# Kernel tuning notes

Hardware: AMD Instinct MI355X
Metric: run time of the kernel (lower is better)

Reference implementation:

```python
import jax, jax.numpy as jnp
import numpy as np

NUM_LAYERS = 4
HIDDEN = 512
HEADS = 8
DK = HIDDEN // HEADS
REPR_IN = 53
REPR_HID = 32
LN_EPS = 1e-5


def _mask_by_1dmask(x, mask):
    # x: [B,H,L,L], mask: [B,L] bool
    pair = mask[:, :, None] & mask[:, None, :]          # [B,L,L]
    masked = jnp.where(pair[:, None, :, :], x, -jnp.inf)
    all_inf = jnp.all(masked == -jnp.inf, axis=-1, keepdims=True)
    return jnp.where(all_inf, 0.0, masked)


def _layernorm(x, g, b):
    mu = jnp.mean(x, axis=-1, keepdims=True)
    var = jnp.mean((x - mu) ** 2, axis=-1, keepdims=True)
    return (x - mu) * jax.lax.rsqrt(var + LN_EPS) * g + b


def _attn_block(x, mask, refCov, Wq, bq, Wk, bk, Wv, bv, Wo, bo,
                Wr1, br1, Wr2, br2, ln_g, ln_b):
    B, L, h = x.shape
    residual = x
    q = (x @ Wq + bq).reshape(B, L, HEADS, DK).transpose(0, 2, 1, 3)  # [B,H,L,dk]
    k = (x @ Wk + bk).reshape(B, L, HEADS, DK).transpose(0, 2, 1, 3)
    v = (x @ Wv + bv).reshape(B, L, HEADS, DK).transpose(0, 2, 1, 3)
    scores = jnp.einsum('bhid,bhjd->bhij', q, k) / np.sqrt(DK).astype(np.float32)
    scores = _mask_by_1dmask(scores, mask)
    attn_w = jax.nn.softmax(scores, axis=-1)
    # per-pair MLP bias: [B,L,L,53] -> [B,L,L,H] -> [B,H,L,L]
    ref = jax.nn.relu(refCov @ Wr1 + br1) @ Wr2 + br2
    ref = ref.transpose(0, 3, 1, 2)
    ref = _mask_by_1dmask(ref, mask)
    ref_w = jax.nn.softmax(ref, axis=-1)
    comb = attn_w + ref_w
    comb = comb / jnp.sum(comb, axis=-1, keepdims=True)
    out = jnp.einsum('bhij,bhjd->bhid', comb, v)
    out = out.transpose(0, 2, 1, 3).reshape(B, L, h)
    out = out @ Wo + bo
    return _layernorm(residual + out, ln_g, ln_b)


def setup_inputs() -> dict:
    key = jax.random.key(0)
    ks = jax.random.split(key, 20)
    B, L = 8, 384
    s = 0.02
    inp = {
        'x': jax.random.normal(ks[0], (B, L, HIDDEN), jnp.float32),
        'mask': jax.random.randint(ks[1], (B, L), 0, 2) > 0,
        'refCov': jax.random.normal(ks[2], (B, L, L, REPR_IN), jnp.float32),
        'Wq': jax.random.normal(ks[3], (NUM_LAYERS, HIDDEN, HIDDEN)) * s,
        'bq': jnp.zeros((NUM_LAYERS, HIDDEN)),
        'Wk': jax.random.normal(ks[4], (NUM_LAYERS, HIDDEN, HIDDEN)) * s,
        'bk': jnp.zeros((NUM_LAYERS, HIDDEN)),
        'Wv': jax.random.normal(ks[5], (NUM_LAYERS, HIDDEN, HIDDEN)) * s,
        'bv': jnp.zeros((NUM_LAYERS, HIDDEN)),
        'Wo': jax.random.normal(ks[6], (NUM_LAYERS, HIDDEN, HIDDEN)) * s,
        'bo': jnp.zeros((NUM_LAYERS, HIDDEN)),
        'Wr1': jax.random.normal(ks[7], (NUM_LAYERS, REPR_IN, REPR_HID)) * 0.1,
        'br1': jnp.zeros((NUM_LAYERS, REPR_HID)),
        'Wr2': jax.random.normal(ks[8], (NUM_LAYERS, REPR_HID, HEADS)) * 0.1,
        'br2': jnp.zeros((NUM_LAYERS, HEADS)),
        'ln_g': jnp.ones((NUM_LAYERS, HIDDEN)),
        'ln_b': jnp.zeros((NUM_LAYERS, HIDDEN)),
        'fn_g': jnp.ones((HIDDEN,)),
        'fn_b': jnp.zeros((HIDDEN,)),
    }
    return inp


def reference(x, mask, refCov, Wq, bq, Wk, bk, Wv, bv, Wo, bo,
              Wr1, br1, Wr2, br2, ln_g, ln_b, fn_g, fn_b):
    # process_node_feature packs flat nodes into [B,L,h] with zeros at padding;
    # equivalent here to zeroing padded positions of x.
    h = x * mask[:, :, None].astype(x.dtype)
    for i in range(NUM_LAYERS):
        h = _attn_block(h, mask, refCov, Wq[i], bq[i], Wk[i], bk[i],
                        Wv[i], bv[i], Wo[i], bo[i], Wr1[i], br1[i],
                        Wr2[i], br2[i], ln_g[i], ln_b[i])
    h = _layernorm(h, fn_g, fn_b)
    return jnp.sum(h * mask[:, :, None].astype(h.dtype), axis=1)  # [B, HIDDEN]
```

## Files before the change

### kernel.cpp

```cpp
#include <hip/hip_runtime.h>
#include <hip/hip_bf16.h>
#include <cstdint>

constexpr int LSEQ  = 384;
constexpr int BATCH = 8;
constexpr int HID   = 512;
constexpr int NHEAD = 8;
constexpr int DKH   = 64;
constexpr int NLAY  = 4;
constexpr int BL    = BATCH * LSEQ;
constexpr int LL2   = LSEQ * LSEQ;
constexpr int BH    = BATCH * NHEAD;

typedef __bf16 bf16x8 __attribute__((ext_vector_type(8)));
typedef float  f32x4  __attribute__((ext_vector_type(4)));
typedef unsigned short ushort_t;

__device__ inline bf16x8 load_frag(const void* p) {
    uint4 u = *reinterpret_cast<const uint4*>(p);
    return __builtin_bit_cast(bf16x8, u);
}
__device__ inline bf16x8 zero_frag() {
    uint4 u = {0u, 0u, 0u, 0u};
    return __builtin_bit_cast(bf16x8, u);
}
__device__ inline f32x4 mfma16(bf16x8 a, bf16x8 b, f32x4 c) {
    return __builtin_amdgcn_mfma_f32_16x16x32_bf16(a, b, c, 0, 0, 0);
}
__device__ inline float b2f(__hip_bfloat16 v) { return __bfloat162float(v); }
__device__ inline ushort_t bfbits(float f) {
    __hip_bfloat16 b = __float2bfloat16(f);
    return *(ushort_t*)&b;
}

__global__ __launch_bounds__(1024) void mask_norm_kernel(
    const unsigned char* __restrict__ raw, unsigned char* __restrict__ m)
{
    __shared__ int fl;
    const int tid = threadIdx.x;
    if (tid == 0) fl = 0;
    __syncthreads();
    int f = 0;
    for (int i = tid; i < BL; i += 1024) {
        const unsigned char v = raw[i];
        if (v > 1) f |= 1;
        if (v && (i & 3)) f |= 2;
        if (v && ((i & 7) == 4)) f |= 4;
        if (v && ((i & 3) <= 1)) f |= 8;
    }
    if (f) atomicOr(&fl, f);
    __syncthreads();
    const int ff = fl;
    int stride, off;
    if (ff & 1) { if (ff & 8) { stride = 2; off = 0; } else { stride = 4; off = 2; } }
    else if (ff & 2) { stride = 1; off = 0; }
    else if (ff & 4) { stride = 4; off = 0; }
    else             { stride = 8; off = 0; }
    for (int i = tid; i < BL; i += 1024)
        m[i] = raw[(size_t)i * stride + off] ? 1 : 0;
}

__global__ __launch_bounds__(256) void wconv_kernel(
    const float* __restrict__ Wq, const float* __restrict__ Wk,
    const float* __restrict__ Wv, const float* __restrict__ Wo,
    ushort_t* __restrict__ WTqkv, ushort_t* __restrict__ WTo)
{
    __shared__ float tile[32][33];
    const int t = blockIdx.x;
    const int ml = t >> 8;
    const int rest = t & 255;
    const int mi = ml >> 2, l = ml & 3;
    const int tk = (rest & 15) * 32;
    const int tn = (rest >> 4) * 32;
    const float* W = (mi == 0) ? Wq : (mi == 1) ? Wk : (mi == 2) ? Wv : Wo;
    const float* src = W + (size_t)l * HID * HID;
    const int c = threadIdx.x & 31, r = threadIdx.x >> 5;
    for (int rr = r; rr < 32; rr += 8)
        tile[rr][c] = src[(size_t)(tk + rr) * HID + tn + c];
    __syncthreads();
    ushort_t* dst = (mi < 3)
        ? WTqkv + ((size_t)l * 1536 + mi * 512) * HID
        : WTo   + (size_t)l * HID * HID;
    for (int rr = r; rr < 32; rr += 8)
        dst[(size_t)(tn + rr) * HID + tk + c] = bfbits(tile[c][rr]);
}

__global__ __launch_bounds__(256) void refw_kernel(
    const float* __restrict__ Wr1, const float* __restrict__ Wr2,
    ushort_t* __restrict__ W1T, ushort_t* __restrict__ W2T)
{
    const int tid = blockIdx.x * 256 + threadIdx.x;
    if (tid < 4 * 32 * 64) {
        const int l = tid >> 11, rem = tid & 2047;
        const int n = rem >> 6, k = rem & 63;
        W1T[tid] = (k < 53) ? bfbits(Wr1[(l * 53 + k) * 32 + n]) : (ushort_t)0;
    } else if (tid < 4 * 32 * 64 + 4 * 16 * 32) {
        const int t2 = tid - 8192;
        const int l = t2 >> 9, rem = t2 & 511;
        const int n = rem >> 5, k = rem & 31;
        W2T[t2] = (n < 8) ? bfbits(Wr2[(l * 32 + k) * 8 + n]) : (ushort_t)0;
    }
}

__global__ __launch_bounds__(256) void pack_kernel(
    const float* __restrict__ x, const unsigned char* __restrict__ mask,
    float* __restrict__ h, __hip_bfloat16* __restrict__ hb)
{
    const int idx = blockIdx.x * 256 + threadIdx.x;
    const int row = idx >> 9;
    const float v = mask[row] ? x[idx] : 0.f;
    h[idx] = v;
    hb[idx] = __float2bfloat16(v);
}

__global__ __launch_bounds__(256) void refmlp_kernel(
    const float* __restrict__ refCov,
    const ushort_t* __restrict__ W1T, const float* __restrict__ br1,
    const ushort_t* __restrict__ W2T, const float* __restrict__ br2,
    __hip_bfloat16* __restrict__ refL)
{
    __shared__ ushort_t smem[256 * 56];

    const int tid = threadIdx.x;
    const int w = tid >> 6, lane = tid & 63;
    const int lr = lane & 15, quad = lane >> 4;
    const size_t p0 = (size_t)blockIdx.x * 256;
    const int b = (int)(p0 / LL2);
    const int rem0 = (int)(p0 - (size_t)b * LL2);

    const float4* src4 = reinterpret_cast<const float4*>(refCov + p0 * 53);
    for (int f = tid; f < 3392; f += 256) {
        float4 v = src4[f];
        const int e = f * 4;
        #pragma unroll
        for (int k = 0; k < 4; ++k) {
            const int g = e + k;
            const int row = g / 53;
            const int col = g - row * 53;
            smem[row * 56 + col] = bfbits(((const float*)&v)[k]);
        }
    }
    smem[tid * 56 + 53] = 0;
    smem[tid * 56 + 54] = 0;
    smem[tid * 56 + 55] = 0;
    __syncthreads();

    bf16x8 afr[4][2];
    #pragma unroll
    for (int mi = 0; mi < 4; ++mi) {
        const ushort_t* rp = smem + (w * 64 + mi * 16 + lr) * 56;
        afr[mi][0] = load_frag(rp + quad * 8);
        afr[mi][1] = (quad < 3) ? load_frag(rp + 32 + quad * 8) : zero_frag();
    }
    __syncthreads();

    ushort_t* C1w = smem + w * 2560;

    #pragma unroll
    for (int l = 0; l < NLAY; ++l) {
        const float bias0 = br1[l * 32 + lr];
        const float bias1 = br1[l * 32 + 16 + lr];
        const float bias2 = br2[l * 8 + (lr & 7)];
        bf16x8 w1f[2][2];
        #pragma unroll
        for (int ni = 0; ni < 2; ++ni)
            #pragma unroll
            for (int ks = 0; ks < 2; ++ks)
                w1f[ni][ks] = load_frag(W1T + ((l * 32 + ni * 16 + lr) * 64) + ks * 32 + quad * 8);
        bf16x8 w2f = load_frag(W2T + (l * 16 + lr) * 32 + quad * 8);

        f32x4 acc[4][2];
        #pragma unroll
        for (int mi = 0; mi < 4; ++mi) {
            acc[mi][0] = (f32x4){bias0, bias0, bias0, bias0};
            acc[mi][1] = (f32x4){bias1, bias1, bias1, bias1};
        }
        #pragma unroll
        for (int mi = 0; mi < 4; ++mi) {
            acc[mi][0] = mfma16(afr[mi][0], w1f[0][0], acc[mi][0]);
            acc[mi][0] = mfma16(afr[mi][1], w1f[0][1], acc[mi][0]);
            acc[mi][1] = mfma16(afr[mi][0], w1f[1][0], acc[mi][1]);
            acc[mi][1] = mfma16(afr[mi][1], w1f[1][1], acc[mi][1]);
        }
        #pragma unroll
        for (int mi = 0; mi < 4; ++mi)
            #pragma unroll
            for (int ni = 0; ni < 2; ++ni)
                #pragma unroll
                for (int r = 0; r < 4; ++r)
                    C1w[(mi * 16 + quad * 4 + r) * 40 + ni * 16 + lr] =
                        bfbits(fmaxf(acc[mi][ni][r], 0.f));

        #pragma unroll
        for (int mi = 0; mi < 4; ++mi) {
            bf16x8 a2 = load_frag(C1w + (mi * 16 + lr) * 40 + quad * 8);
            f32x4 a = (f32x4){bias2, bias2, bias2, bias2};
            a = mfma16(a2, w2f, a);
            if (lr < 8) {
                uint2 pk;
                pk.x = (unsigned)bfbits(a[0]) | ((unsigned)bfbits(a[1]) << 16);
                pk.y = (unsigned)bfbits(a[2]) | ((unsigned)bfbits(a[3]) << 16);
                const size_t plane = ((size_t)(l * 8 + b) * 8 + lr) * LL2;
                *reinterpret_cast<uint2*>((ushort_t*)refL + plane + rem0 +
                                          w * 64 + mi * 16 + quad * 4) = pk;
            }
        }
    }
}

__global__ __launch_bounds__(256) void gemm_qkv_kernel(
    const __hip_bfloat16* __restrict__ A,
    const __hip_bfloat16* __restrict__ BT,
    const float* __restrict__ bq, const float* __restrict__ bk,
    const float* __restrict__ bv,
    __hip_bfloat16* __restrict__ q, __hip_bfloat16* __restrict__ kk,
    __hip_bfloat16* __restrict__ vT)
{
    const int bm = blockIdx.x % (BL / 64);
    const int bn = blockIdx.x / (BL / 64);
    const int wv = threadIdx.x >> 6;
    const int lane = threadIdx.x & 63;
    const int lr = lane & 15, quad = lane >> 4;
    const int m0 = bm * 64 + (wv & 1) * 32;
    const int n0g = bn * 64 + (wv >> 1) * 32;
    f32x4 acc[2][2];
    #pragma unroll
    for (int i = 0; i < 2; ++i)
        #pragma unroll
        for (int j = 0; j < 2; ++j) acc[i][j] = (f32x4){0.f, 0.f, 0.f, 0.f};
    const __hip_bfloat16* a0p = A + (size_t)(m0 + lr) * HID;
    const __hip_bfloat16* a1p = A + (size_t)(m0 + 16 + lr) * HID;
    const __hip_bfloat16* b0p = BT + (size_t)(n0g + lr) * HID;
    const __hip_bfloat16* b1p = BT + (size_t)(n0g + 16 + lr) * HID;
    #pragma unroll 4
    for (int k0 = 0; k0 < HID; k0 += 32) {
        const int ka = k0 + quad * 8;
        bf16x8 a0 = load_frag(a0p + ka);
        bf16x8 a1 = load_frag(a1p + ka);
        bf16x8 b0 = load_frag(b0p + ka);
        bf16x8 b1 = load_frag(b1p + ka);
        acc[0][0] = mfma16(a0, b0, acc[0][0]);
        acc[0][1] = mfma16(a0, b1, acc[0][1]);
        acc[1][0] = mfma16(a1, b0, acc[1][0]);
        acc[1][1] = mfma16(a1, b1, acc[1][1]);
    }
    const int mat = n0g >> 9;
    const float* bias = (mat == 0) ? bq : (mat == 1) ? bk : bv;
    const float scale = (mat == 0) ? 0.125f : 1.0f;
    __hip_bfloat16* outp = (mat == 0) ? q : (mat == 1) ? kk : vT;
    #pragma unroll
    for (int mi = 0; mi < 2; ++mi)
        #pragma unroll
        for (int ni = 0; ni < 2; ++ni)
            #pragma unroll
            for (int r = 0; r < 4; ++r) {
                const int m = m0 + mi * 16 + quad * 4 + r;
                const int ng = n0g + ni * 16 + lr;
                const int n = ng & 511;
                float v = (acc[mi][ni][r] + bias[n]) * scale;
                const int bb = m / LSEQ, ii = m % LSEQ;
                const int hh = n >> 6, d = n & 63;
                if (mat == 2)
                    outp[((size_t)(bb * NHEAD + hh) * DKH + d) * LSEQ + ii] = __float2bfloat16(v);
                else
                    outp[((size_t)(bb * NHEAD + hh) * LSEQ + ii) * DKH + d] = __float2bfloat16(v);
            }
}

__global__ __launch_bounds__(256) void gemm_oproj_kernel(
    const __hip_bfloat16* __restrict__ A,
    const __hip_bfloat16* __restrict__ BT,
    const float* __restrict__ bias,
    float* __restrict__ outf)
{
    const int bm = blockIdx.x % (BL / 64);
    const int bn = blockIdx.x / (BL / 64);
    const int wv = threadIdx.x >> 6;
    const int lane = threadIdx.x & 63;
    const int lr = lane & 15, quad = lane >> 4;
    const int m0 = bm * 64 + (wv & 1) * 32;
    const int n0 = bn * 64 + (wv >> 1) * 32;
    f32x4 acc[2][2];
    #pragma unroll
    for (int i = 0; i < 2; ++i)
        #pragma unroll
        for (int j = 0; j < 2; ++j) acc[i][j] = (f32x4){0.f, 0.f, 0.f, 0.f};
    const __hip_bfloat16* a0p = A + (size_t)(m0 + lr) * HID;
    const __hip_bfloat16* a1p = A + (size_t)(m0 + 16 + lr) * HID;
    const __hip_bfloat16* b0p = BT + (size_t)(n0 + lr) * HID;
    const __hip_bfloat16* b1p = BT + (size_t)(n0 + 16 + lr) * HID;
    #pragma unroll 4
    for (int k0 = 0; k0 < HID; k0 += 32) {
        const int ka = k0 + quad * 8;
        bf16x8 a0 = load_frag(a0p + ka);
        bf16x8 a1 = load_frag(a1p + ka);
        bf16x8 b0 = load_frag(b0p + ka);
        bf16x8 b1 = load_frag(b1p + ka);
        acc[0][0] = mfma16(a0, b0, acc[0][0]);
        acc[0][1] = mfma16(a0, b1, acc[0][1]);
        acc[1][0] = mfma16(a1, b0, acc[1][0]);
        acc[1][1] = mfma16(a1, b1, acc[1][1]);
    }
    #pragma unroll
    for (int mi = 0; mi < 2; ++mi)
        #pragma unroll
        for (int ni = 0; ni < 2; ++ni)
            #pragma unroll
            for (int r = 0; r < 4; ++r) {
                const int m = m0 + mi * 16 + quad * 4 + r;
                const int n = n0 + ni * 16 + lr;
                outf[(size_t)m * HID + n] = acc[mi][ni][r] + bias[n];
            }
}

__global__ __launch_bounds__(256) void attn_fused_kernel(
    const __hip_bfloat16* __restrict__ Q,
    const __hip_bfloat16* __restrict__ Km,
    const __hip_bfloat16* __restrict__ VT,
    const __hip_bfloat16* __restrict__ refl,
    const unsigned char* __restrict__ mask,
    __hip_bfloat16* __restrict__ AO)
{
    __shared__ __align__(16) ushort_t Pl[32 * 392];
    __shared__ float redm_s[2][2][16], redm_r[2][2][16];
    __shared__ float reds_s[2][2][16], reds_r[2][2][16];

    const int bh = blockIdx.x / 12;
    const int i0 = (blockIdx.x % 12) * 32;
    const int b  = bh >> 3, hh = bh & 7;
    const int w = threadIdx.x >> 6, lane = threadIdx.x & 63;
    const int s = w & 1, h2 = w >> 1;
    const int lr = lane & 15, quad = lane >> 4;

    const __hip_bfloat16* qb = Q  + (size_t)bh * LSEQ * DKH;
    const __hip_bfloat16* kb = Km + (size_t)bh * LSEQ * DKH;
    const unsigned char* mrow = mask + b * LSEQ;

    f32x4 acc[12];
    #pragma unroll
    for (int nt = 0; nt < 12; ++nt) acc[nt] = (f32x4){0.f, 0.f, 0.f, 0.f};
    #pragma unroll
    for (int k0 = 0; k0 < DKH; k0 += 32) {
        const int ka = k0 + quad * 8;
        bf16x8 a = load_frag(qb + (size_t)(i0 + s * 16 + lr) * DKH + ka);
        #pragma unroll
        for (int nt = 0; nt < 12; ++nt) {
            bf16x8 bf = load_frag(kb + (size_t)(h2 * 192 + nt * 16 + lr) * DKH + ka);
            acc[nt] = mfma16(a, bf, acc[nt]);
        }
    }

    bool vm[12];
    #pragma unroll
    for (int nt = 0; nt < 12; ++nt)
        vm[nt] = mrow[h2 * 192 + nt * 16 + lr] != 0;

    const __hip_bfloat16* rbase = refl + (size_t)bh * LL2 +
                                  (size_t)(i0 + s * 16) * LSEQ + h2 * 192;
    float rv[12][4];
    #pragma unroll
    for (int nt = 0; nt < 12; ++nt)
        #pragma unroll
        for (int r = 0; r < 4; ++r)
            rv[nt][r] = b2f(rbase[(size_t)(quad * 4 + r) * LSEQ + nt * 16 + lr]);

    float ms[4], mr2[4];
    #pragma unroll
    for (int r = 0; r < 4; ++r) { ms[r] = -1e30f; mr2[r] = -1e30f; }
    #pragma unroll
    for (int nt = 0; nt < 12; ++nt)
        #pragma unroll
        for (int r = 0; r < 4; ++r) {
            acc[nt][r] = vm[nt] ? acc[nt][r] : -1e30f;
            rv[nt][r]  = vm[nt] ? rv[nt][r]  : -1e30f;
            ms[r]  = fmaxf(ms[r],  acc[nt][r]);
            mr2[r] = fmaxf(mr2[r], rv[nt][r]);
        }
    #pragma unroll
    for (int off = 8; off > 0; off >>= 1)
        #pragma unroll
        for (int r = 0; r < 4; ++r) {
            ms[r]  = fmaxf(ms[r],  __shfl_xor(ms[r],  off));
            mr2[r] = fmaxf(mr2[r], __shfl_xor(mr2[r], off));
        }
    if (lr == 0)
        #pragma unroll
        for (int r = 0; r < 4; ++r) {
            redm_s[s][h2][quad * 4 + r] = ms[r];
            redm_r[s][h2][quad * 4 + r] = mr2[r];
        }
    __syncthreads();
    #pragma unroll
    for (int r = 0; r < 4; ++r) {
        ms[r]  = fmaxf(redm_s[s][0][quad * 4 + r], redm_s[s][1][quad * 4 + r]);
        mr2[r] = fmaxf(redm_r[s][0][quad * 4 + r], redm_r[s][1][quad * 4 + r]);
    }

    float Ss[4] = {0.f, 0.f, 0.f, 0.f}, Sr[4] = {0.f, 0.f, 0.f, 0.f};
    #pragma unroll
    for (int nt = 0; nt < 12; ++nt)
        #pragma unroll
        for (int r = 0; r < 4; ++r) {
            acc[nt][r] = __expf(acc[nt][r] - ms[r]);  Ss[r] += acc[nt][r];
            rv[nt][r]  = __expf(rv[nt][r]  - mr2[r]); Sr[r] += rv[nt][r];
        }
    #pragma unroll
    for (int off = 8; off > 0; off >>= 1)
        #pragma unroll
        for (int r = 0; r < 4; ++r) {
            Ss[r] += __shfl_xor(Ss[r], off);
            Sr[r] += __shfl_xor(Sr[r], off);
        }
    if (lr == 0)
        #pragma unroll
        for (int r = 0; r < 4; ++r) {
            reds_s[s][h2][quad * 4 + r] = Ss[r];
            reds_r[s][h2][quad * 4 + r] = Sr[r];
        }
    __syncthreads();

    float cs[4], cr[4], rm[4];
    #pragma unroll
    for (int r = 0; r < 4; ++r) {
        const float SsF = reds_s[s][0][quad * 4 + r] + reds_s[s][1][quad * 4 + r];
        const float SrF = reds_r[s][0][quad * 4 + r] + reds_r[s][1][quad * 4 + r];
        cs[r] = 0.5f / SsF;
        cr[r] = 0.5f / SrF;
        rm[r] = mrow[i0 + s * 16 + quad * 4 + r] ? 1.f : 0.f;
    }
    #pragma unroll
    for (int nt = 0; nt < 12; ++nt)
        #pragma unroll
        for (int r = 0; r < 4; ++r)
            Pl[(s * 16 + quad * 4 + r) * 392 + h2 * 192 + nt * 16 + lr] =
                bfbits((acc[nt][r] * cs[r] + rv[nt][r] * cr[r]) * rm[r]);
    __syncthreads();

    const __hip_bfloat16* vb = VT + (size_t)bh * DKH * LSEQ;
    f32x4 oa[2];
    oa[0] = (f32x4){0.f, 0.f, 0.f, 0.f};
    oa[1] = (f32x4){0.f, 0.f, 0.f, 0.f};
    #pragma unroll 4
    for (int k0 = 0; k0 < LSEQ; k0 += 32) {
        const int ka = k0 + quad * 8;
        bf16x8 a = load_frag(Pl + (s * 16 + lr) * 392 + ka);
        #pragma unroll
        for (int dt = 0; dt < 2; ++dt) {
            bf16x8 bf = load_frag(vb + (size_t)(h2 * 32 + dt * 16 + lr) * LSEQ + ka);
            oa[dt] = mfma16(a, bf, oa[dt]);
        }
    }
    #pragma unroll
    for (int dt = 0; dt < 2; ++dt)
        #pragma unroll
        for (int r = 0; r < 4; ++r)
            AO[(size_t)(b * LSEQ + i0 + s * 16 + quad * 4 + r) * HID +
               hh * DKH + h2 * 32 + dt * 16 + lr] = __float2bfloat16(oa[dt][r]);
}

__global__ __launch_bounds__(256) void ln_kernel(
    const float* __restrict__ resid, const float* __restrict__ proj,
    const float* __restrict__ g, const float* __restrict__ beta,
    float* __restrict__ outf, __hip_bfloat16* __restrict__ outb,
    const unsigned char* __restrict__ mask, int flags)
{
    const int row = blockIdx.x, tid = threadIdx.x;
    const size_t base = (size_t)row * HID;
    float x0 = resid[base + tid], x1 = resid[base + tid + 256];
    if (flags & 1) { x0 += proj[base + tid]; x1 += proj[base + tid + 256]; }
    float s = x0 + x1, s2 = x0 * x0 + x1 * x1;
    #pragma unroll
    for (int off = 32; off > 0; off >>= 1) {
        s += __shfl_xor(s, off);
        s2 += __shfl_xor(s2, off);
    }
    __shared__ float rs[4], rs2[4];
    if ((tid & 63) == 0) { rs[tid >> 6] = s; rs2[tid >> 6] = s2; }
    __syncthreads();
    s = rs[0] + rs[1] + rs[2] + rs[3];
    s2 = rs2[0] + rs2[1] + rs2[2] + rs2[3];
    const float mu = s * (1.f / HID);
    const float var = s2 * (1.f / HID) - mu * mu;
    const float rstd = rsqrtf(var + 1e-5f);
    float y0 = (x0 - mu) * rstd * g[tid] + beta[tid];
    float y1 = (x1 - mu) * rstd * g[tid + 256] + beta[tid + 256];
    if ((flags & 2) && !mask[row]) { y0 = 0.f; y1 = 0.f; }
    outf[base + tid] = y0;
    outf[base + tid + 256] = y1;
    if (flags & 4) {
        outb[base + tid] = __float2bfloat16(y0);
        outb[base + tid + 256] = __float2bfloat16(y1);
    }
}

__global__ __launch_bounds__(512) void reduce_kernel(
    const float* __restrict__ hf, float* __restrict__ out)
{
    const int b = blockIdx.x, c = threadIdx.x;
    float s = 0.f;
    for (int i = 0; i < LSEQ; ++i)
        s += hf[((size_t)(b * LSEQ + i)) * HID + c];
    out[b * HID + c] = s;
}

extern "C" void kernel_launch(void* const* d_in, const int* in_sizes, int n_in,
                              void* d_out, int out_size, void* d_ws, size_t ws_size,
                              hipStream_t stream)
{
    const float* x   = (const float*)d_in[0];
    const unsigned char* mraw = (const unsigned char*)d_in[1];
    const float* refCov = (const float*)d_in[2];
    const float* Wq = (const float*)d_in[3];
    const float* bq = (const float*)d_in[4];
    const float* Wk = (const float*)d_in[5];
    const float* bk = (const float*)d_in[6];
    const float* Wv = (const float*)d_in[7];
    const float* bv = (const float*)d_in[8];
    const float* Wo = (const float*)d_in[9];
    const float* bo = (const float*)d_in[10];
    const float* Wr1 = (const float*)d_in[11];
    const float* br1 = (const float*)d_in[12];
    const float* Wr2 = (const float*)d_in[13];
    const float* br2 = (const float*)d_in[14];
    const float* ln_g = (const float*)d_in[15];
    const float* ln_b = (const float*)d_in[16];
    const float* fn_g = (const float*)d_in[17];
    const float* fn_b = (const float*)d_in[18];
    float* outp = (float*)d_out;

    char* ws = (char*)d_ws;
    size_t off = 0;
    auto alloc = [&](size_t bytes) -> char* {
        char* p = ws + off;
        off += (bytes + 255) & ~(size_t)255;
        return p;
    };
    __hip_bfloat16* refL  = (__hip_bfloat16*)alloc((size_t)NLAY * BH * LL2 * 2);
    float*          h     = (float*)alloc((size_t)BL * HID * 4);
    __hip_bfloat16* hb    = (__hip_bfloat16*)alloc((size_t)BL * HID * 2);
    __hip_bfloat16* q     = (__hip_bfloat16*)alloc((size_t)BH * LSEQ * DKH * 2);
    __hip_bfloat16* kk    = (__hip_bfloat16*)alloc((size_t)BH * LSEQ * DKH * 2);
    __hip_bfloat16* vT    = (__hip_bfloat16*)alloc((size_t)BH * DKH * LSEQ * 2);
    float*          S     = (float*)alloc((size_t)BH * LL2 * 4);
    __hip_bfloat16* AO    = (__hip_bfloat16*)alloc((size_t)BL * HID * 2);
    float*          proj  = (float*)alloc((size_t)BL * HID * 4);
    ushort_t*       WTqkv = (ushort_t*)alloc((size_t)NLAY * 1536 * HID * 2);
    ushort_t*       WTo   = (ushort_t*)alloc((size_t)NLAY * HID * HID * 2);
    ushort_t*       W1T   = (ushort_t*)alloc((size_t)4 * 32 * 64 * 2);
    ushort_t*       W2T   = (ushort_t*)alloc((size_t)4 * 16 * 32 * 2);
    unsigned char*  msk   = (unsigned char*)alloc(BL);
    float*          hfin  = S;

    mask_norm_kernel<<<1, 1024, 0, stream>>>(mraw, msk);
    wconv_kernel<<<4096, 256, 0, stream>>>(Wq, Wk, Wv, Wo, WTqkv, WTo);
    refw_kernel<<<40, 256, 0, stream>>>(Wr1, Wr2, W1T, W2T);
    pack_kernel<<<6144, 256, 0, stream>>>(x, msk, h, hb);
    refmlp_kernel<<<4608, 256, 0, stream>>>(refCov, W1T, br1, W2T, br2, refL);

    for (int l = 0; l < NLAY; ++l) {
        const __hip_bfloat16* WTl = (const __hip_bfloat16*)(WTqkv + (size_t)l * 1536 * HID);
        const __hip_bfloat16* WTol = (const __hip_bfloat16*)(WTo + (size_t)l * HID * HID);
        gemm_qkv_kernel<<<1152, 256, 0, stream>>>(hb, WTl, bq + l * HID, bk + l * HID,
                                                  bv + l * HID, q, kk, vT);
        attn_fused_kernel<<<768, 256, 0, stream>>>(q, kk, vT,
                                                   refL + (size_t)l * BH * LL2, msk, AO);
        gemm_oproj_kernel<<<384, 256, 0, stream>>>(AO, WTol, bo + l * HID, proj);
        ln_kernel<<<3072, 256, 0, stream>>>(h, proj, ln_g + l * HID, ln_b + l * HID,
                                            h, hb, nullptr, 1 | 4);
    }
    ln_kernel<<<3072, 256, 0, stream>>>(h, nullptr, fn_g, fn_b, hfin, nullptr, msk, 2);
    reduce_kernel<<<8, 512, 0, stream>>>(hfin, outp);
}
```

Before: 840.2 us.

## Split attention block across eight waves instead of four

The fused attention kernel now launches 512 threads per block. The key dimension is split four ways (96 columns per wave) instead of two, and each wave produces 16 output dims instead of 32. This halves per-thread register arrays (score and ref tiles), which may raise occupancy and latency hiding for the ref loads. The cost is wider cross-wave reductions through shared memory, more waves syncing per block, and each Q fragment being loaded by more waves.

Result: no change. 830.0 us (-1.2%).

```diff
diff --git a/kernel.cpp b/kernel.cpp
--- a/kernel.cpp
+++ b/kernel.cpp
@@ -313,7 +313,7 @@
             }
 }
 
-__global__ __launch_bounds__(256) void attn_fused_kernel(
+__global__ __launch_bounds__(512) void attn_fused_kernel(
     const __hip_bfloat16* __restrict__ Q,
     const __hip_bfloat16* __restrict__ Km,
     const __hip_bfloat16* __restrict__ VT,
@@ -322,44 +322,44 @@
     __hip_bfloat16* __restrict__ AO)
 {
     __shared__ __align__(16) ushort_t Pl[32 * 392];
-    __shared__ float redm_s[2][2][16], redm_r[2][2][16];
-    __shared__ float reds_s[2][2][16], reds_r[2][2][16];
+    __shared__ float redm_s[2][4][16], redm_r[2][4][16];
+    __shared__ float reds_s[2][4][16], reds_r[2][4][16];
 
     const int bh = blockIdx.x / 12;
     const int i0 = (blockIdx.x % 12) * 32;
     const int b  = bh >> 3, hh = bh & 7;
     const int w = threadIdx.x >> 6, lane = threadIdx.x & 63;
-    const int s = w & 1, h2 = w >> 1;
+    const int s = w & 1, h4 = w >> 1;
     const int lr = lane & 15, quad = lane >> 4;
 
     const __hip_bfloat16* qb = Q  + (size_t)bh * LSEQ * DKH;
     const __hip_bfloat16* kb = Km + (size_t)bh * LSEQ * DKH;
     const unsigned char* mrow = mask + b * LSEQ;
 
-    f32x4 acc[12];
-    #pragma unroll
-    for (int nt = 0; nt < 12; ++nt) acc[nt] = (f32x4){0.f, 0.f, 0.f, 0.f};
+    f32x4 acc[6];
+    #pragma unroll
+    for (int nt = 0; nt < 6; ++nt) acc[nt] = (f32x4){0.f, 0.f, 0.f, 0.f};
     #pragma unroll
     for (int k0 = 0; k0 < DKH; k0 += 32) {
         const int ka = k0 + quad * 8;
         bf16x8 a = load_frag(qb + (size_t)(i0 + s * 16 + lr) * DKH + ka);
         #pragma unroll
-        for (int nt = 0; nt < 12; ++nt) {
-            bf16x8 bf = load_frag(kb + (size_t)(h2 * 192 + nt * 16 + lr) * DKH + ka);
+        for (int nt = 0; nt < 6; ++nt) {
+            bf16x8 bf = load_frag(kb + (size_t)(h4 * 96 + nt * 16 + lr) * DKH + ka);
             acc[nt] = mfma16(a, bf, acc[nt]);
         }
     }
 
-    bool vm[12];
-    #pragma unroll
-    for (int nt = 0; nt < 12; ++nt)
-        vm[nt] = mrow[h2 * 192 + nt * 16 + lr] != 0;
+    bool vm[6];
+    #pragma unroll
+    for (int nt = 0; nt < 6; ++nt)
+        vm[nt] = mrow[h4 * 96 + nt * 16 + lr] != 0;
 
     const __hip_bfloat16* rbase = refl + (size_t)bh * LL2 +
-                                  (size_t)(i0 + s * 16) * LSEQ + h2 * 192;
-    float rv[12][4];
-    #pragma unroll
-    for (int nt = 0; nt < 12; ++nt)
+                                  (size_t)(i0 + s * 16) * LSEQ + h4 * 96;
+    float rv[6][4];
+    #pragma unroll
+    for (int nt = 0; nt < 6; ++nt)
         #pragma unroll
         for (int r = 0; r < 4; ++r)
             rv[nt][r] = b2f(rbase[(size_t)(quad * 4 + r) * LSEQ + nt * 16 + lr]);
@@ -368,7 +368,7 @@
     #pragma unroll
     for (int r = 0; r < 4; ++r) { ms[r] = -1e30f; mr2[r] = -1e30f; }
     #pragma unroll
-    for (int nt = 0; nt < 12; ++nt)
+    for (int nt = 0; nt < 6; ++nt)
         #pragma unroll
         for (int r = 0; r < 4; ++r) {
             acc[nt][r] = vm[nt] ? acc[nt][r] : -1e30f;
@@ -386,19 +386,22 @@
     if (lr == 0)
         #pragma unroll
         for (int r = 0; r < 4; ++r) {
-            redm_s[s][h2][quad * 4 + r] = ms[r];
-            redm_r[s][h2][quad * 4 + r] = mr2[r];
+            redm_s[s][h4][quad * 4 + r] = ms[r];
+            redm_r[s][h4][quad * 4 + r] = mr2[r];
         }
     __syncthreads();
     #pragma unroll
     for (int r = 0; r < 4; ++r) {
-        ms[r]  = fmaxf(redm_s[s][0][quad * 4 + r], redm_s[s][1][quad * 4 + r]);
-        mr2[r] = fmaxf(redm_r[s][0][quad * 4 + r], redm_r[s][1][quad * 4 + r]);
+        const int x = quad * 4 + r;
+        ms[r]  = fmaxf(fmaxf(redm_s[s][0][x], redm_s[s][1][x]),
+                       fmaxf(redm_s[s][2][x], redm_s[s][3][x]));
+        mr2[r] = fmaxf(fmaxf(redm_r[s][0][x], redm_r[s][1][x]),
+                       fmaxf(redm_r[s][2][x], redm_r[s][3][x]));
     }
 
     float Ss[4] = {0.f, 0.f, 0.f, 0.f}, Sr[4] = {0.f, 0.f, 0.f, 0.f};
     #pragma unroll
-    for (int nt = 0; nt < 12; ++nt)
+    for (int nt = 0; nt < 6; ++nt)
         #pragma unroll
         for (int r = 0; r < 4; ++r) {
             acc[nt][r] = __expf(acc[nt][r] - ms[r]);  Ss[r] += acc[nt][r];
@@ -414,48 +417,44 @@
     if (lr == 0)
         #pragma unroll
         for (int r = 0; r < 4; ++r) {
-            reds_s[s][h2][quad * 4 + r] = Ss[r];
-            reds_r[s][h2][quad * 4 + r] = Sr[r];
+            reds_s[s][h4][quad * 4 + r] = Ss[r];
+            reds_r[s][h4][quad * 4 + r] = Sr[r];
         }
     __syncthreads();
 
     float cs[4], cr[4], rm[4];
     #pragma unroll
     for (int r = 0; r < 4; ++r) {
-        const float SsF = reds_s[s][0][quad * 4 + r] + reds_s[s][1][quad * 4 + r];
-        const float SrF = reds_r[s][0][quad * 4 + r] + reds_r[s][1][quad * 4 + r];
+        const int x = quad * 4 + r;
+        const float SsF = reds_s[s][0][x] + reds_s[s][1][x] +
+                          reds_s[s][2][x] + reds_s[s][3][x];
+        const float SrF = reds_r[s][0][x] + reds_r[s][1][x] +
+                          reds_r[s][2][x] + reds_r[s][3][x];
         cs[r] = 0.5f / SsF;
         cr[r] = 0.5f / SrF;
-        rm[r] = mrow[i0 + s * 16 + quad * 4 + r] ? 1.f : 0.f;
-    }
-    #pragma unroll
-    for (int nt = 0; nt < 12; ++nt)
+        rm[r] = mrow[i0 + s * 16 + x] ? 1.f : 0.f;
+    }
+    #pragma unroll
+    for (int nt = 0; nt < 6; ++nt)
         #pragma unroll
         for (int r = 0; r < 4; ++r)
-            Pl[(s * 16 + quad * 4 + r) * 392 + h2 * 192 + nt * 16 + lr] =
+            Pl[(s * 16 + quad * 4 + r) * 392 + h4 * 96 + nt * 16 + lr] =
                 bfbits((acc[nt][r] * cs[r] + rv[nt][r] * cr[r]) * rm[r]);
     __syncthreads();
 
     const __hip_bfloat16* vb = VT + (size_t)bh * DKH * LSEQ;
-    f32x4 oa[2];
-    oa[0] = (f32x4){0.f, 0.f, 0.f, 0.f};
-    oa[1] = (f32x4){0.f, 0.f, 0.f, 0.f};
+    f32x4 oa = (f32x4){0.f, 0.f, 0.f, 0.f};
     #pragma unroll 4
     for (int k0 = 0; k0 < LSEQ; k0 += 32) {
         const int ka = k0 + quad * 8;
         bf16x8 a = load_frag(Pl + (s * 16 + lr) * 392 + ka);
-        #pragma unroll
-        for (int dt = 0; dt < 2; ++dt) {
-            bf16x8 bf = load_frag(vb + (size_t)(h2 * 32 + dt * 16 + lr) * LSEQ + ka);
-            oa[dt] = mfma16(a, bf, oa[dt]);
-        }
-    }
-    #pragma unroll
-    for (int dt = 0; dt < 2; ++dt)
-        #pragma unroll
-        for (int r = 0; r < 4; ++r)
-            AO[(size_t)(b * LSEQ + i0 + s * 16 + quad * 4 + r) * HID +
-               hh * DKH + h2 * 32 + dt * 16 + lr] = __float2bfloat16(oa[dt][r]);
+        bf16x8 bf = load_frag(vb + (size_t)(h4 * 16 + lr) * LSEQ + ka);
+        oa = mfma16(a, bf, oa);
+    }
+    #pragma unroll
+    for (int r = 0; r < 4; ++r)
+        AO[(size_t)(b * LSEQ + i0 + s * 16 + quad * 4 + r) * HID +
+           hh * DKH + h4 * 16 + lr] = __float2bfloat16(oa[r]);
 }
 
 __global__ __launch_bounds__(256) void ln_kernel(
@@ -562,7 +561,7 @@
         const __hip_bfloat16* WTol = (const __hip_bfloat16*)(WTo + (size_t)l * HID * HID);
         gemm_qkv_kernel<<<1152, 256, 0, stream>>>(hb, WTl, bq + l * HID, bk + l * HID,
                                                   bv + l * HID, q, kk, vT);
-        attn_fused_kernel<<<768, 256, 0, stream>>>(q, kk, vT,
+        attn_fused_kernel<<<768, 512, 0, stream>>>(q, kk, vT,
                                                    refL + (size_t)l * BH * LL2, msk, AO);
         gemm_oproj_kernel<<<384, 256, 0, stream>>>(AO, WTol, bo + l * HID, proj);
         ln_kernel<<<3072, 256, 0, stream>>>(h, proj, ln_g + l * HID, ln_b + l * HID,
```
